# Kernel optimization log

Measured on AMD Instinct MI355X. Metric: run time of the kernel, lower is better.

## Reference

```python
import jax, jax.numpy as jnp
import numpy as np

B, N, D = 16, 2048, 128
SCALE = 1.0 / np.sqrt(D).astype(np.float32)


def setup_inputs() -> dict:
    key = jax.random.key(0)
    ks = jax.random.split(key, 9)
    Q = jax.random.normal(ks[0], (B, N, D), dtype=jnp.float32)
    K = jax.random.normal(ks[1], (B, N, D), dtype=jnp.float32)
    V = jax.random.normal(ks[2], (B, N, D), dtype=jnp.float32)
    bias_dis = 0.1 * jax.random.normal(ks[3], (N, N), dtype=jnp.float32)
    bias_dtw = 0.1 * jax.random.normal(ks[4], (N, N), dtype=jnp.float32)
    bias_pattern = 0.1 * jax.random.normal(ks[5], (N, N), dtype=jnp.float32)
    bias_poi = 0.1 * jax.random.normal(ks[6], (N, N), dtype=jnp.float32)
    # key/query padding masks: mostly True (valid) with some padding
    input_mask = jax.random.randint(ks[7], (B, N), 0, 10) > 0
    embeddings_mask = jax.random.randint(ks[8], (B, N), 0, 10) > 0
    # lower-triangular causal mask (diagonal kept so every row has a valid key)
    causal_mask = jnp.tril(jnp.ones((N, N), dtype=bool))
    return {"Q": Q, "K": K, "V": V, "bias_dis": bias_dis, "bias_dtw": bias_dtw,
            "bias_pattern": bias_pattern, "bias_poi": bias_poi,
            "input_mask": input_mask, "embeddings_mask": embeddings_mask,
            "causal_mask": causal_mask}


def reference(Q, K, V, bias_dis, bias_dtw, bias_pattern, bias_poi,
              input_mask, embeddings_mask, causal_mask):
    # masked_fill_(~mask, 0.0) on K, V with input_mask[:, :, None]
    km = input_mask[:, :, None]
    K = jnp.where(km, K, 0.0)
    V = jnp.where(km, V, 0.0)
    # masked_fill_(~mask, 0.0) on Q with embeddings_mask[:, :, None]
    Q = jnp.where(embeddings_mask[:, :, None], Q, 0.0)
    # scores [B, N, N] = Q K^T / sqrt(dim)
    scores = jnp.einsum('bnd,bmd->bnm', Q, K) * SCALE
    # causal masked_fill_(~causal_mask, -inf)
    scores = jnp.where(causal_mask[None, :, :], scores, -jnp.inf)
    # per-batch bias loop == broadcast add of summed [N, N] biases
    scores = scores + (bias_dis + bias_dtw + bias_pattern + bias_poi)[None, :, :]
    P = jax.nn.softmax(scores, axis=-1)
    # dropout p=0 (eval) -> identity
    return jnp.einsum('bnm,bmd->bnd', P, V)
```

## Files before the change

### kernel.cpp

```cpp
#include <hip/hip_runtime.h>
#include <math.h>

constexpr int Bc = 16;
constexpr int Nc = 2048;
constexpr int Dc = 128;
constexpr int NCHUNK = Nc / 64;
constexpr float SCALE_F = 0.08838834764831845f;

typedef __bf16 bf16x8 __attribute__((ext_vector_type(8)));
typedef __bf16 bf16x4 __attribute__((ext_vector_type(4)));
typedef float  f32x4  __attribute__((ext_vector_type(4)));

constexpr size_t KPACK_BYTES = (size_t)Bc * NCHUNK * 16 * 64 * 16;
constexpr size_t VPACK_BYTES = KPACK_BYTES;
constexpr size_t BIAS_BYTES  = (size_t)Nc * Nc * 4;
constexpr int CHUNK_ELEMS = 16 * 64 * 8;

template<int CTRL>
__device__ __forceinline__ float dpp_mv(float v) {
    return __builtin_bit_cast(float,
        __builtin_amdgcn_update_dpp(0, __builtin_bit_cast(int, v),
                                    CTRL, 0xF, 0xF, true));
}
__device__ __forceinline__ float rmax16(float v) {
    v = fmaxf(v, dpp_mv<0xB1>(v));
    v = fmaxf(v, dpp_mv<0x4E>(v));
    v = fmaxf(v, dpp_mv<0x141>(v));
    v = fmaxf(v, dpp_mv<0x140>(v));
    return v;
}
__device__ __forceinline__ float rsum16(float v) {
    v += dpp_mv<0xB1>(v);
    v += dpp_mv<0x4E>(v);
    v += dpp_mv<0x141>(v);
    v += dpp_mv<0x140>(v);
    return v;
}

__global__ __launch_bounds__(256) void prep_fused(
    const float* __restrict__ K, const float* __restrict__ V,
    const int* __restrict__ imask,
    const float* __restrict__ b0, const float* __restrict__ b1,
    const float* __restrict__ b2, const float* __restrict__ b3,
    __bf16* __restrict__ Kp, __bf16* __restrict__ Vp, float* __restrict__ bs)
{
    __shared__ __align__(16) __bf16 Ks[64][136];
    __shared__ __align__(16) __bf16 Vs[64][136];
    const int bid = blockIdx.x;
    const int tid = threadIdx.x;

    if (bid >= 512) {
        const int i = (bid - 512) * 256 + tid;
        const float4 a = ((const float4*)b0)[i];
        const float4 c = ((const float4*)b1)[i];
        const float4 d = ((const float4*)b2)[i];
        const float4 e = ((const float4*)b3)[i];
        float4 r;
        r.x = a.x + c.x + d.x + e.x;
        r.y = a.y + c.y + d.y + e.y;
        r.z = a.z + c.z + d.z + e.z;
        r.w = a.w + c.w + d.w + e.w;
        ((float4*)bs)[i] = r;
        return;
    }

    const int c = bid & 31;
    const int b = bid >> 5;
    const int m0 = c * 64;
    const float* Kb = K + (size_t)b * Nc * Dc;
    const float* Vb = V + (size_t)b * Nc * Dc;
    const int* imb = imask + b * Nc;

    #pragma unroll
    for (int it = 0; it < 8; ++it) {
        const int idx = it * 256 + tid;
        const int row = idx >> 5;
        const int c4  = idx & 31;
        const int gm  = m0 + row;
        const float msk = imb[gm] ? 1.0f : 0.0f;
        const float4 kf = ((const float4*)(Kb + (size_t)gm * Dc))[c4];
        const float4 vf = ((const float4*)(Vb + (size_t)gm * Dc))[c4];
        bf16x4 kb, vb;
        kb[0] = (__bf16)(kf.x * msk); kb[1] = (__bf16)(kf.y * msk);
        kb[2] = (__bf16)(kf.z * msk); kb[3] = (__bf16)(kf.w * msk);
        vb[0] = (__bf16)(vf.x * msk); vb[1] = (__bf16)(vf.y * msk);
        vb[2] = (__bf16)(vf.z * msk); vb[3] = (__bf16)(vf.w * msk);
        *(bf16x4*)&Ks[row][c4 * 4] = kb;
        *(bf16x4*)&Vs[row][c4 * 4] = vb;
    }
    __syncthreads();

    const size_t chunk_base = (size_t)(b * NCHUNK + c) * CHUNK_ELEMS;
    #pragma unroll
    for (int i = 0; i < 4; ++i) {
        const int s = i * 256 + tid;
        const int f = s >> 6;
        const int l = s & 63;
        const int quad = (l >> 4) & 3;
        const int l15  = l & 15;
        {
            const int jt = f >> 2, kd = f & 3;
            const bf16x8 kv = *(const bf16x8*)&Ks[jt * 16 + l15][kd * 32 + quad * 8];
            *(bf16x8*)&Kp[chunk_base + (size_t)f * 512 + l * 8] = kv;
        }
        {
            const int kj = f >> 3, dt = f & 7;
            bf16x8 vv;
            #pragma unroll
            for (int j = 0; j < 8; ++j)
                vv[j] = Vs[kj * 32 + quad * 8 + j][dt * 16 + l15];
            *(bf16x8*)&Vp[chunk_base + (size_t)f * 512 + l * 8] = vv;
        }
    }
}

__global__ __launch_bounds__(128, 2) void attn_wave(
    const float* __restrict__ Q,
    const __bf16* __restrict__ Kp, const __bf16* __restrict__ Vp,
    const float* __restrict__ bias, const int* __restrict__ emask,
    float* __restrict__ out)
{
    __shared__ __align__(16) __bf16 Pl[2][32][72];
    __shared__ __align__(16) float  Olds[128][36];
    __shared__ float Ml[32];
    __shared__ float Ll[32];

    const int tid  = threadIdx.x;
    const int w    = tid >> 6;
    const int lane = tid & 63;
    const int quad = lane >> 4;
    const int l15  = lane & 15;
    const int b = blockIdx.x;
    const int y = blockIdx.y;
    const int t = (y < 32) ? y : ((y < 48) ? (79 - y) : (111 - y));
    const int r0 = t * 32;
    const int C  = (t >> 1) + 1;

    const float*  Qb  = Q  + (size_t)b * Nc * Dc;
    const __bf16* Kpb = Kp + (size_t)b * NCHUNK * CHUNK_ELEMS;
    const __bf16* Vpb = Vp + (size_t)b * NCHUNK * CHUNK_ELEMS;

    bf16x8 qf[2][4];
    #pragma unroll
    for (int h = 0; h < 2; ++h) {
        const int row = r0 + h * 16 + l15;
        const float qs = emask[b * Nc + row] ? SCALE_F : 0.0f;
        const float4* qr = (const float4*)(Qb + (size_t)row * Dc);
        #pragma unroll
        for (int kd = 0; kd < 4; ++kd) {
            const float4 xx = qr[kd * 8 + quad * 2];
            const float4 yy = qr[kd * 8 + quad * 2 + 1];
            qf[h][kd][0] = (__bf16)(xx.x * qs); qf[h][kd][1] = (__bf16)(xx.y * qs);
            qf[h][kd][2] = (__bf16)(xx.z * qs); qf[h][kd][3] = (__bf16)(xx.w * qs);
            qf[h][kd][4] = (__bf16)(yy.x * qs); qf[h][kd][5] = (__bf16)(yy.y * qs);
            qf[h][kd][6] = (__bf16)(yy.z * qs); qf[h][kd][7] = (__bf16)(yy.w * qs);
        }
    }

    const float* bp[2][4];
    #pragma unroll
    for (int h = 0; h < 2; ++h)
        #pragma unroll
        for (int reg = 0; reg < 4; ++reg)
            bp[h][reg] = bias + (size_t)(r0 + h * 16 + quad * 4 + reg) * Nc + l15;

    f32x4 oacc[2][8];
    float mrun[2][4], lrun[2][4];
    #pragma unroll
    for (int h = 0; h < 2; ++h) {
        #pragma unroll
        for (int dt = 0; dt < 8; ++dt) {
            oacc[h][dt][0] = 0.f; oacc[h][dt][1] = 0.f;
            oacc[h][dt][2] = 0.f; oacc[h][dt][3] = 0.f;
        }
        #pragma unroll
        for (int reg = 0; reg < 4; ++reg) { mrun[h][reg] = -INFINITY; lrun[h][reg] = 0.f; }
    }

    for (int c = w; c < C; c += 2) {
        float bc[2][4][4];
        #pragma unroll
        for (int h = 0; h < 2; ++h)
            #pragma unroll
            for (int jt = 0; jt < 4; ++jt)
                #pragma unroll
                for (int reg = 0; reg < 4; ++reg)
                    bc[h][jt][reg] = __builtin_nontemporal_load(bp[h][reg] + c * 64 + jt * 16);

        const size_t off = (size_t)c * CHUNK_ELEMS;

        f32x4 sc[2][4];
        #pragma unroll
        for (int h = 0; h < 2; ++h)
            #pragma unroll
            for (int jt = 0; jt < 4; ++jt) {
                sc[h][jt][0] = 0.f; sc[h][jt][1] = 0.f;
                sc[h][jt][2] = 0.f; sc[h][jt][3] = 0.f;
            }
        #pragma unroll
        for (int jt = 0; jt < 4; ++jt)
            #pragma unroll
            for (int kd = 0; kd < 4; ++kd) {
                const bf16x8 kf = *(const bf16x8*)&Kpb[off + (size_t)(jt * 4 + kd) * 512 + lane * 8];
                sc[0][jt] = __builtin_amdgcn_mfma_f32_16x16x32_bf16(qf[0][kd], kf, sc[0][jt], 0, 0, 0);
                sc[1][jt] = __builtin_amdgcn_mfma_f32_16x16x32_bf16(qf[1][kd], kf, sc[1][jt], 0, 0, 0);
            }

        if (c == C - 1) {
            #pragma unroll
            for (int h = 0; h < 2; ++h)
                #pragma unroll
                for (int jt = 0; jt < 4; ++jt)
                    #pragma unroll
                    for (int reg = 0; reg < 4; ++reg) {
                        const int gr = r0 + h * 16 + quad * 4 + reg;
                        const int gc = c * 64 + jt * 16 + l15;
                        const float v = sc[h][jt][reg] + bc[h][jt][reg];
                        sc[h][jt][reg] = (gc > gr) ? -INFINITY : v;
                    }
        } else {
            #pragma unroll
            for (int h = 0; h < 2; ++h)
                #pragma unroll
                for (int jt = 0; jt < 4; ++jt)
                    #pragma unroll
                    for (int reg = 0; reg < 4; ++reg)
                        sc[h][jt][reg] += bc[h][jt][reg];
        }

        #pragma unroll
        for (int h = 0; h < 2; ++h) {
            float mx[4];
            int grow = 0;
            #pragma unroll
            for (int reg = 0; reg < 4; ++reg) {
                float m = fmaxf(fmaxf(sc[h][0][reg], sc[h][1][reg]),
                                fmaxf(sc[h][2][reg], sc[h][3][reg]));
                m = rmax16(m);
                mx[reg] = m;
                grow |= (m > mrun[h][reg]);
            }
            if (__any(grow)) {
                #pragma unroll
                for (int reg = 0; reg < 4; ++reg) {
                    const float mn = fmaxf(mrun[h][reg], mx[reg]);
                    const float alpha = __expf(mrun[h][reg] - mn);
                    mrun[h][reg] = mn;
                    lrun[h][reg] *= alpha;
                    #pragma unroll
                    for (int dt = 0; dt < 8; ++dt) oacc[h][dt][reg] *= alpha;
                }
            }
            #pragma unroll
            for (int reg = 0; reg < 4; ++reg) {
                float ls = 0.f;
                #pragma unroll
                for (int jt = 0; jt < 4; ++jt) {
                    const float pv = __expf(sc[h][jt][reg] - mrun[h][reg]);
                    sc[h][jt][reg] = pv;
                    ls += pv;
                }
                lrun[h][reg] += rsum16(ls);
                #pragma unroll
                for (int jt = 0; jt < 4; ++jt)
                    Pl[w][h * 16 + quad * 4 + reg][jt * 16 + l15] = (__bf16)sc[h][jt][reg];
            }
        }

        #pragma unroll
        for (int kj = 0; kj < 2; ++kj) {
            const bf16x8 pa0 = *(const bf16x8*)&Pl[w][l15][kj * 32 + quad * 8];
            const bf16x8 pa1 = *(const bf16x8*)&Pl[w][16 + l15][kj * 32 + quad * 8];
            #pragma unroll
            for (int dt = 0; dt < 8; ++dt) {
                const bf16x8 vf = *(const bf16x8*)&Vpb[off + (size_t)(kj * 8 + dt) * 512 + lane * 8];
                oacc[0][dt] = __builtin_amdgcn_mfma_f32_16x16x32_bf16(pa0, vf, oacc[0][dt], 0, 0, 0);
                oacc[1][dt] = __builtin_amdgcn_mfma_f32_16x16x32_bf16(pa1, vf, oacc[1][dt], 0, 0, 0);
            }
        }
    }

    if (w == 1) {
        #pragma unroll
        for (int h = 0; h < 2; ++h) {
            #pragma unroll
            for (int dt = 0; dt < 8; ++dt)
                *(f32x4*)&Olds[dt * 16 + l15][h * 16 + quad * 4] = oacc[h][dt];
            if (l15 == 0) {
                #pragma unroll
                for (int reg = 0; reg < 4; ++reg) {
                    Ml[h * 16 + quad * 4 + reg] = mrun[h][reg];
                    Ll[h * 16 + quad * 4 + reg] = lrun[h][reg];
                }
            }
        }
    }
    __syncthreads();
    if (w == 0) {
        #pragma unroll
        for (int h = 0; h < 2; ++h) {
            float a0[4], a1[4], linv[4];
            #pragma unroll
            for (int reg = 0; reg < 4; ++reg) {
                const int rr = h * 16 + quad * 4 + reg;
                const float m1 = Ml[rr];
                const float l1 = Ll[rr];
                const float m  = fmaxf(mrun[h][reg], m1);
                a0[reg] = __expf(mrun[h][reg] - m);
                a1[reg] = __expf(m1 - m);
                linv[reg] = 1.0f / (lrun[h][reg] * a0[reg] + l1 * a1[reg]);
            }
            #pragma unroll
            for (int dt = 0; dt < 8; ++dt) {
                const f32x4 o1 = *(const f32x4*)&Olds[dt * 16 + l15][h * 16 + quad * 4];
                #pragma unroll
                for (int reg = 0; reg < 4; ++reg) {
                    const int gr = r0 + h * 16 + quad * 4 + reg;
                    const float v = (oacc[h][dt][reg] * a0[reg] + o1[reg] * a1[reg]) * linv[reg];
                    __builtin_nontemporal_store(v, out + ((size_t)b * Nc + gr) * Dc + dt * 16 + l15);
                }
            }
        }
    }
}

__global__ __launch_bounds__(256) void attn_mfma_legacy(
    const float* __restrict__ Q, const float* __restrict__ K, const float* __restrict__ V,
    const float* __restrict__ p0, const float* __restrict__ p1,
    const float* __restrict__ p2, const float* __restrict__ p3,
    const int* __restrict__ imask, const int* __restrict__ emask,
    float* __restrict__ out)
{
    __shared__ __align__(16) __bf16 Klds[64][136];
    __shared__ __align__(16) __bf16 Vt[128][72];
    __shared__ __align__(16) __bf16 Plds[4][16][72];
    const int tid  = threadIdx.x;
    const int w    = tid >> 6;
    const int lane = tid & 63;
    const int quad = lane >> 4;
    const int l15  = lane & 15;
    const int b = blockIdx.y;
    const int x = blockIdx.x, yy = blockIdx.y;
    const int ti = (yy < 8) ? x : (31 - x);
    const int q0 = ti * 64, q0w = q0 + w * 16;
    const float* Qb = Q + (size_t)b * Nc * Dc;
    const float* Kb = K + (size_t)b * Nc * Dc;
    const float* Vb = V + (size_t)b * Nc * Dc;
    const int* imb = imask + b * Nc;

    bf16x8 qfrag[4];
    {
        const int row = q0w + l15;
        const float qs = emask[b * Nc + row] ? SCALE_F : 0.0f;
        const float4* qr = (const float4*)(Qb + (size_t)row * Dc);
        #pragma unroll
        for (int kd = 0; kd < 4; ++kd) {
            const float4 xv = qr[kd * 8 + quad * 2];
            const float4 yv = qr[kd * 8 + quad * 2 + 1];
            qfrag[kd][0]=(__bf16)(xv.x*qs); qfrag[kd][1]=(__bf16)(xv.y*qs);
            qfrag[kd][2]=(__bf16)(xv.z*qs); qfrag[kd][3]=(__bf16)(xv.w*qs);
            qfrag[kd][4]=(__bf16)(yv.x*qs); qfrag[kd][5]=(__bf16)(yv.y*qs);
            qfrag[kd][6]=(__bf16)(yv.z*qs); qfrag[kd][7]=(__bf16)(yv.w*qs);
        }
    }
    f32x4 oacc[8];
    #pragma unroll
    for (int dt = 0; dt < 8; ++dt){oacc[dt][0]=0.f;oacc[dt][1]=0.f;oacc[dt][2]=0.f;oacc[dt][3]=0.f;}
    float mrun[4]={-INFINITY,-INFINITY,-INFINITY,-INFINITY}, lrun[4]={0.f,0.f,0.f,0.f};

    for (int m0 = 0; m0 <= q0; m0 += 64) {
        __syncthreads();
        #pragma unroll
        for (int it = 0; it < 8; ++it) {
            const int idx = it * 256 + tid;
            const int row = idx >> 5, c4 = idx & 31;
            const int gm = m0 + row;
            const float msk = imb[gm] ? 1.0f : 0.0f;
            const float4 kf = ((const float4*)(Kb + (size_t)gm * Dc))[c4];
            const float4 vf = ((const float4*)(Vb + (size_t)gm * Dc))[c4];
            bf16x4 kb;
            kb[0]=(__bf16)(kf.x*msk); kb[1]=(__bf16)(kf.y*msk);
            kb[2]=(__bf16)(kf.z*msk); kb[3]=(__bf16)(kf.w*msk);
            *(bf16x4*)&Klds[row][c4*4] = kb;
            Vt[c4*4+0][row]=(__bf16)(vf.x*msk); Vt[c4*4+1][row]=(__bf16)(vf.y*msk);
            Vt[c4*4+2][row]=(__bf16)(vf.z*msk); Vt[c4*4+3][row]=(__bf16)(vf.w*msk);
        }
        __syncthreads();
        f32x4 sc[4];
        #pragma unroll
        for (int jt = 0; jt < 4; ++jt){sc[jt][0]=0.f;sc[jt][1]=0.f;sc[jt][2]=0.f;sc[jt][3]=0.f;}
        #pragma unroll
        for (int jt = 0; jt < 4; ++jt)
            #pragma unroll
            for (int kd = 0; kd < 4; ++kd) {
                const bf16x8 bfr = *(const bf16x8*)&Klds[jt*16+l15][kd*32+quad*8];
                sc[jt] = __builtin_amdgcn_mfma_f32_16x16x32_bf16(qfrag[kd], bfr, sc[jt], 0, 0, 0);
            }
        #pragma unroll
        for (int jt = 0; jt < 4; ++jt)
            #pragma unroll
            for (int reg = 0; reg < 4; ++reg) {
                const int gr = q0w + quad*4 + reg;
                const int gc = m0 + jt*16 + l15;
                const size_t boff = (size_t)gr * Nc + gc;
                const float bsx = p0[boff] + p1[boff] + p2[boff] + p3[boff];
                const float v = sc[jt][reg] + bsx;
                sc[jt][reg] = (gc > gr) ? -INFINITY : v;
            }
        #pragma unroll
        for (int reg = 0; reg < 4; ++reg) {
            float mx = fmaxf(fmaxf(sc[0][reg], sc[1][reg]), fmaxf(sc[2][reg], sc[3][reg]));
            mx = rmax16(mx);
            const float mn = fmaxf(mrun[reg], mx);
            const float alpha = __expf(mrun[reg] - mn);
            mrun[reg] = mn; lrun[reg] *= alpha;
            #pragma unroll
            for (int dt = 0; dt < 8; ++dt) oacc[dt][reg] *= alpha;
            float ls = 0.f;
            #pragma unroll
            for (int jt = 0; jt < 4; ++jt) {
                const float pv = __expf(sc[jt][reg] - mn);
                sc[jt][reg] = pv; ls += pv;
            }
            lrun[reg] += rsum16(ls);
        }
        #pragma unroll
        for (int jt = 0; jt < 4; ++jt)
            #pragma unroll
            for (int reg = 0; reg < 4; ++reg)
                Plds[w][quad*4+reg][jt*16+l15] = (__bf16)sc[jt][reg];
        #pragma unroll
        for (int kj = 0; kj < 2; ++kj) {
            const bf16x8 pa = *(const bf16x8*)&Plds[w][l15][kj*32+quad*8];
            #pragma unroll
            for (int dt = 0; dt < 8; ++dt) {
                const bf16x8 vb = *(const bf16x8*)&Vt[dt*16+l15][kj*32+quad*8];
                oacc[dt] = __builtin_amdgcn_mfma_f32_16x16x32_bf16(pa, vb, oacc[dt], 0, 0, 0);
            }
        }
    }
    #pragma unroll
    for (int reg = 0; reg < 4; ++reg) {
        const float inv = 1.0f / lrun[reg];
        const int gr = q0w + quad*4 + reg;
        float* orow = out + ((size_t)b * Nc + gr) * Dc;
        #pragma unroll
        for (int dt = 0; dt < 8; ++dt)
            orow[dt*16+l15] = oacc[dt][reg] * inv;
    }
}

extern "C" void kernel_launch(void* const* d_in, const int* in_sizes, int n_in,
                              void* d_out, int out_size, void* d_ws, size_t ws_size,
                              hipStream_t stream) {
    const float* Q  = (const float*)d_in[0];
    const float* K  = (const float*)d_in[1];
    const float* V  = (const float*)d_in[2];
    const float* b0 = (const float*)d_in[3];
    const float* b1 = (const float*)d_in[4];
    const float* b2 = (const float*)d_in[5];
    const float* b3 = (const float*)d_in[6];
    const int* im   = (const int*)d_in[7];
    const int* em   = (const int*)d_in[8];
    float* out      = (float*)d_out;

    if (ws_size >= KPACK_BYTES + VPACK_BYTES + BIAS_BYTES) {
        __bf16* Kp = (__bf16*)d_ws;
        __bf16* Vp = (__bf16*)((char*)d_ws + KPACK_BYTES);
        float*  bs = (float*)((char*)d_ws + KPACK_BYTES + VPACK_BYTES);
        prep_fused<<<512 + (Nc * Nc / 4) / 256, 256, 0, stream>>>(
            K, V, im, b0, b1, b2, b3, Kp, Vp, bs);
        attn_wave<<<dim3(Bc, 64), 128, 0, stream>>>(Q, Kp, Vp, bs, em, out);
    } else {
        attn_mfma_legacy<<<dim3(NCHUNK, Bc), 256, 0, stream>>>(
            Q, K, V, b0, b1, b2, b3, im, em, out);
    }
}
```

Measured before the change: 248.2 us.

## Pack causal bias tiles in MFMA layout and split KV chunks across four waves

The prep kernel now sums the four biases only for the causal (lower-triangular) 32x64 tiles and stores each tile pre-permuted in the MFMA accumulator layout. The attention kernel can then initialise the score accumulators with one coalesced vector load instead of scattered nontemporal scalar loads. The attention block grows from 2 to 4 waves, each taking every fourth KV chunk, with a sequential LDS merge of the partial softmax states. This roughly halves bias traffic and adds parallelism per block, at the cost of extra barriers, a serial merge chain and higher register and LDS pressure per block.

```diff
diff --git a/kernel.cpp b/kernel.cpp
--- a/kernel.cpp
+++ b/kernel.cpp
@@ -13,8 +13,14 @@
 
 constexpr size_t KPACK_BYTES = (size_t)Bc * NCHUNK * 16 * 64 * 16;
 constexpr size_t VPACK_BYTES = KPACK_BYTES;
-constexpr size_t BIAS_BYTES  = (size_t)Nc * Nc * 4;
+constexpr int NUNITS = 1056;
+constexpr size_t BIASP_BYTES = (size_t)NUNITS * 2048 * 4;
 constexpr int CHUNK_ELEMS = 16 * 64 * 8;
+
+__device__ __forceinline__ int ftri(int t) {
+    const int m = t >> 1;
+    return (t & 1) ? (m + 1) * (m + 1) : m * (m + 1);
+}
 
 template<int CTRL>
 __device__ __forceinline__ float dpp_mv(float v) {
@@ -42,25 +48,53 @@
     const int* __restrict__ imask,
     const float* __restrict__ b0, const float* __restrict__ b1,
     const float* __restrict__ b2, const float* __restrict__ b3,
-    __bf16* __restrict__ Kp, __bf16* __restrict__ Vp, float* __restrict__ bs)
+    __bf16* __restrict__ Kp, __bf16* __restrict__ Vp, float* __restrict__ bsp)
 {
     __shared__ __align__(16) __bf16 Ks[64][136];
     __shared__ __align__(16) __bf16 Vs[64][136];
+    __shared__ __align__(16) float  Ts[32][68];
     const int bid = blockIdx.x;
     const int tid = threadIdx.x;
 
     if (bid >= 512) {
-        const int i = (bid - 512) * 256 + tid;
-        const float4 a = ((const float4*)b0)[i];
-        const float4 c = ((const float4*)b1)[i];
-        const float4 d = ((const float4*)b2)[i];
-        const float4 e = ((const float4*)b3)[i];
-        float4 r;
-        r.x = a.x + c.x + d.x + e.x;
-        r.y = a.y + c.y + d.y + e.y;
-        r.z = a.z + c.z + d.z + e.z;
-        r.w = a.w + c.w + d.w + e.w;
-        ((float4*)bs)[i] = r;
+        const int u = bid - 512;
+        int t = 0;
+        while (ftri(t + 1) <= u) ++t;
+        const int c = u - ftri(t);
+
+        #pragma unroll
+        for (int i = 0; i < 2; ++i) {
+            const int v = tid + 256 * i;
+            const int row = v >> 4, c4 = v & 15;
+            const size_t g = (size_t)(t * 32 + row) * Nc + c * 64 + c4 * 4;
+            const float4 a = *(const float4*)(b0 + g);
+            const float4 d = *(const float4*)(b1 + g);
+            const float4 e = *(const float4*)(b2 + g);
+            const float4 f = *(const float4*)(b3 + g);
+            float4 s;
+            s.x = a.x + d.x + e.x + f.x;
+            s.y = a.y + d.y + e.y + f.y;
+            s.z = a.z + d.z + e.z + f.z;
+            s.w = a.w + d.w + e.w + f.w;
+            *(float4*)&Ts[row][c4 * 4] = s;
+        }
+        __syncthreads();
+
+        const int lane = tid >> 2;
+        const int quad = lane >> 4, l15 = lane & 15;
+        const int k0 = (tid & 3) * 8;
+        float* outp = bsp + (size_t)u * 2048;
+        #pragma unroll
+        for (int g2 = 0; g2 < 2; ++g2) {
+            const int k = k0 + g2 * 4;
+            const int h = (k >> 4) & 1, jt = (k >> 2) & 3;
+            float4 o;
+            o.x = Ts[h * 16 + quad * 4 + 0][jt * 16 + l15];
+            o.y = Ts[h * 16 + quad * 4 + 1][jt * 16 + l15];
+            o.z = Ts[h * 16 + quad * 4 + 2][jt * 16 + l15];
+            o.w = Ts[h * 16 + quad * 4 + 3][jt * 16 + l15];
+            ((float4*)outp)[tid * 2 + g2] = o;
+        }
         return;
     }
 
@@ -114,13 +148,13 @@
     }
 }
 
-__global__ __launch_bounds__(128, 2) void attn_wave(
+__global__ __launch_bounds__(256, 3) void attn_split(
     const float* __restrict__ Q,
     const __bf16* __restrict__ Kp, const __bf16* __restrict__ Vp,
-    const float* __restrict__ bias, const int* __restrict__ emask,
+    const float* __restrict__ biasp, const int* __restrict__ emask,
     float* __restrict__ out)
 {
-    __shared__ __align__(16) __bf16 Pl[2][32][72];
+    __shared__ __align__(16) __bf16 Pl[4][32][72];
     __shared__ __align__(16) float  Olds[128][36];
     __shared__ float Ml[32];
     __shared__ float Ll[32];
@@ -135,6 +169,8 @@
     const int t = (y < 32) ? y : ((y < 48) ? (79 - y) : (111 - y));
     const int r0 = t * 32;
     const int C  = (t >> 1) + 1;
+    const int mh = t >> 1;
+    const int fbase = (t & 1) ? (mh + 1) * (mh + 1) : mh * (mh + 1);
 
     const float*  Qb  = Q  + (size_t)b * Nc * Dc;
     const __bf16* Kpb = Kp + (size_t)b * NCHUNK * CHUNK_ELEMS;
@@ -157,13 +193,6 @@
         }
     }
 
-    const float* bp[2][4];
-    #pragma unroll
-    for (int h = 0; h < 2; ++h)
-        #pragma unroll
-        for (int reg = 0; reg < 4; ++reg)
-            bp[h][reg] = bias + (size_t)(r0 + h * 16 + quad * 4 + reg) * Nc + l15;
-
     f32x4 oacc[2][8];
     float mrun[2][4], lrun[2][4];
     #pragma unroll
@@ -177,31 +206,22 @@
         for (int reg = 0; reg < 4; ++reg) { mrun[h][reg] = -INFINITY; lrun[h][reg] = 0.f; }
     }
 
-    for (int c = w; c < C; c += 2) {
-        float bc[2][4][4];
+    for (int c = w; c < C; c += 4) {
+        const __bf16* kc = Kpb + (size_t)c * CHUNK_ELEMS;
+        const __bf16* vc = Vpb + (size_t)c * CHUNK_ELEMS;
+        const f32x4* bpp = (const f32x4*)(biasp + (size_t)(fbase + c) * 2048) + lane * 8;
+
+        f32x4 sc[2][4];
         #pragma unroll
         for (int h = 0; h < 2; ++h)
             #pragma unroll
             for (int jt = 0; jt < 4; ++jt)
-                #pragma unroll
-                for (int reg = 0; reg < 4; ++reg)
-                    bc[h][jt][reg] = __builtin_nontemporal_load(bp[h][reg] + c * 64 + jt * 16);
-
-        const size_t off = (size_t)c * CHUNK_ELEMS;
-
-        f32x4 sc[2][4];
-        #pragma unroll
-        for (int h = 0; h < 2; ++h)
-            #pragma unroll
-            for (int jt = 0; jt < 4; ++jt) {
-                sc[h][jt][0] = 0.f; sc[h][jt][1] = 0.f;
-                sc[h][jt][2] = 0.f; sc[h][jt][3] = 0.f;
-            }
+                sc[h][jt] = bpp[h * 4 + jt];
         #pragma unroll
         for (int jt = 0; jt < 4; ++jt)
             #pragma unroll
             for (int kd = 0; kd < 4; ++kd) {
-                const bf16x8 kf = *(const bf16x8*)&Kpb[off + (size_t)(jt * 4 + kd) * 512 + lane * 8];
+                const bf16x8 kf = *(const bf16x8*)&kc[(size_t)(jt * 4 + kd) * 512 + lane * 8];
                 sc[0][jt] = __builtin_amdgcn_mfma_f32_16x16x32_bf16(qf[0][kd], kf, sc[0][jt], 0, 0, 0);
                 sc[1][jt] = __builtin_amdgcn_mfma_f32_16x16x32_bf16(qf[1][kd], kf, sc[1][jt], 0, 0, 0);
             }
@@ -215,17 +235,8 @@
                     for (int reg = 0; reg < 4; ++reg) {
                         const int gr = r0 + h * 16 + quad * 4 + reg;
                         const int gc = c * 64 + jt * 16 + l15;
-                        const float v = sc[h][jt][reg] + bc[h][jt][reg];
-                        sc[h][jt][reg] = (gc > gr) ? -INFINITY : v;
+                        if (gc > gr) sc[h][jt][reg] = -INFINITY;
                     }
-        } else {
-            #pragma unroll
-            for (int h = 0; h < 2; ++h)
-                #pragma unroll
-                for (int jt = 0; jt < 4; ++jt)
-                    #pragma unroll
-                    for (int reg = 0; reg < 4; ++reg)
-                        sc[h][jt][reg] += bc[h][jt][reg];
         }
 
         #pragma unroll
@@ -273,14 +284,14 @@
             const bf16x8 pa1 = *(const bf16x8*)&Pl[w][16 + l15][kj * 32 + quad * 8];
             #pragma unroll
             for (int dt = 0; dt < 8; ++dt) {
-                const bf16x8 vf = *(const bf16x8*)&Vpb[off + (size_t)(kj * 8 + dt) * 512 + lane * 8];
+                const bf16x8 vf = *(const bf16x8*)&vc[(size_t)(kj * 8 + dt) * 512 + lane * 8];
                 oacc[0][dt] = __builtin_amdgcn_mfma_f32_16x16x32_bf16(pa0, vf, oacc[0][dt], 0, 0, 0);
                 oacc[1][dt] = __builtin_amdgcn_mfma_f32_16x16x32_bf16(pa1, vf, oacc[1][dt], 0, 0, 0);
             }
         }
     }
 
-    if (w == 1) {
+    auto write_partial = [&]() {
         #pragma unroll
         for (int h = 0; h < 2; ++h) {
             #pragma unroll
@@ -294,31 +305,50 @@
                 }
             }
         }
-    }
+    };
+    auto merge_lds = [&]() {
+        #pragma unroll
+        for (int h = 0; h < 2; ++h) {
+            float aw[4], al[4];
+            #pragma unroll
+            for (int reg = 0; reg < 4; ++reg) {
+                const int rr = h * 16 + quad * 4 + reg;
+                const float mL = Ml[rr], lL = Ll[rr];
+                const float m = fmaxf(mrun[h][reg], mL);
+                const float mm = (m == -INFINITY) ? 0.0f : m;
+                aw[reg] = __expf(mrun[h][reg] - mm);
+                al[reg] = __expf(mL - mm);
+                mrun[h][reg] = m;
+                lrun[h][reg] = lrun[h][reg] * aw[reg] + lL * al[reg];
+            }
+            #pragma unroll
+            for (int dt = 0; dt < 8; ++dt) {
+                const f32x4 o = *(const f32x4*)&Olds[dt * 16 + l15][h * 16 + quad * 4];
+                #pragma unroll
+                for (int reg = 0; reg < 4; ++reg)
+                    oacc[h][dt][reg] = oacc[h][dt][reg] * aw[reg] + o[reg] * al[reg];
+            }
+        }
+    };
+
+    if (w == 3) write_partial();
+    __syncthreads();
+    if (w == 2) { merge_lds(); write_partial(); }
+    __syncthreads();
+    if (w == 1) { merge_lds(); write_partial(); }
     __syncthreads();
     if (w == 0) {
+        merge_lds();
         #pragma unroll
         for (int h = 0; h < 2; ++h) {
-            float a0[4], a1[4], linv[4];
             #pragma unroll
             for (int reg = 0; reg < 4; ++reg) {
-                const int rr = h * 16 + quad * 4 + reg;
-                const float m1 = Ml[rr];
-                const float l1 = Ll[rr];
-                const float m  = fmaxf(mrun[h][reg], m1);
-                a0[reg] = __expf(mrun[h][reg] - m);
-                a1[reg] = __expf(m1 - m);
-                linv[reg] = 1.0f / (lrun[h][reg] * a0[reg] + l1 * a1[reg]);
-            }
-            #pragma unroll
-            for (int dt = 0; dt < 8; ++dt) {
-                const f32x4 o1 = *(const f32x4*)&Olds[dt * 16 + l15][h * 16 + quad * 4];
-                #pragma unroll
-                for (int reg = 0; reg < 4; ++reg) {
-                    const int gr = r0 + h * 16 + quad * 4 + reg;
-                    const float v = (oacc[h][dt][reg] * a0[reg] + o1[reg] * a1[reg]) * linv[reg];
-                    __builtin_nontemporal_store(v, out + ((size_t)b * Nc + gr) * Dc + dt * 16 + l15);
-                }
+                const float inv = 1.0f / lrun[h][reg];
+                const int gr = r0 + h * 16 + quad * 4 + reg;
+                float* orow = out + ((size_t)b * Nc + gr) * Dc;
+                #pragma unroll
+                for (int dt = 0; dt < 8; ++dt)
+                    __builtin_nontemporal_store(oacc[h][dt][reg] * inv, orow + dt * 16 + l15);
             }
         }
     }
@@ -464,13 +494,13 @@
     const int* em   = (const int*)d_in[8];
     float* out      = (float*)d_out;
 
-    if (ws_size >= KPACK_BYTES + VPACK_BYTES + BIAS_BYTES) {
-        __bf16* Kp = (__bf16*)d_ws;
-        __bf16* Vp = (__bf16*)((char*)d_ws + KPACK_BYTES);
-        float*  bs = (float*)((char*)d_ws + KPACK_BYTES + VPACK_BYTES);
-        prep_fused<<<512 + (Nc * Nc / 4) / 256, 256, 0, stream>>>(
-            K, V, im, b0, b1, b2, b3, Kp, Vp, bs);
-        attn_wave<<<dim3(Bc, 64), 128, 0, stream>>>(Q, Kp, Vp, bs, em, out);
+    if (ws_size >= KPACK_BYTES + VPACK_BYTES + BIASP_BYTES) {
+        __bf16* Kp  = (__bf16*)d_ws;
+        __bf16* Vp  = (__bf16*)((char*)d_ws + KPACK_BYTES);
+        float*  bsp = (float*)((char*)d_ws + KPACK_BYTES + VPACK_BYTES);
+        prep_fused<<<512 + NUNITS, 256, 0, stream>>>(
+            K, V, im, b0, b1, b2, b3, Kp, Vp, bsp);
+        attn_split<<<dim3(Bc, 64), 256, 0, stream>>>(Q, Kp, Vp, bsp, em, out);
     } else {
         attn_mfma_legacy<<<dim3(NCHUNK, Bc), 256, 0, stream>>>(
             Q, K, V, b0, b1, b2, b3, im, em, out);
```

Result: no change. 246.7 us (-0.6%).
